# Optimization experiments

Measured on AMD Instinct MI355X. Metric: run time of the kernel, lower is better.

## Reference

```python
import jax, jax.numpy as jnp
import numpy as np

B, T, D_IN, D_OUT, N_HEAD = 2, 2048, 1024, 1024, 16
HEAD_DIM = D_OUT // N_HEAD


def setup_inputs() -> dict:
    key = jax.random.key(0)
    k1, k2, k3, k4 = jax.random.split(key, 4)
    s = 0.02  # init scale for weights
    return {
        "x": jax.random.normal(k1, (B, T, D_IN), jnp.float32),
        "Wq": jax.random.normal(k2, (D_OUT, D_IN), jnp.float32) * s,
        "Wk": jax.random.normal(k3, (D_OUT, D_IN), jnp.float32) * s,
        "Wv": jax.random.normal(k4, (D_OUT, D_IN), jnp.float32) * s,
    }


def reference(x, Wq, Wk, Wv):
    b, t, _ = x.shape
    h, hd = N_HEAD, HEAD_DIM
    # Linear projections (torch Linear: x @ W.T), split heads -> [b,h,t,hd]
    q = (x @ Wq.T).reshape(b, t, h, hd).transpose(0, 2, 1, 3)
    k = (x @ Wk.T).reshape(b, t, h, hd).transpose(0, 2, 1, 3)
    v = (x @ Wv.T).reshape(b, t, h, hd).transpose(0, 2, 1, 3)
    # raw scores [b,h,t,t], causal mask BEFORE scaling (as in source)
    omega = jnp.einsum("bhqd,bhkd->bhqk", q, k)
    causal = jnp.triu(jnp.ones((t, t), dtype=bool), k=1)
    omega = jnp.where(causal, -jnp.inf, omega)
    attw = jax.nn.softmax(omega / jnp.sqrt(jnp.asarray(hd, omega.dtype)), axis=-1)
    ctx = jnp.einsum("bhqk,bhkd->bhqd", attw, v)  # [b,h,t,hd]
    # Faithful to source: transpose(2,3) then view(B,T,d_out)
    out = jnp.swapaxes(ctx, 2, 3).reshape(b, t, D_OUT)
    return out
```

## Files before the change

kernel.cpp:

```cpp
#include <hip/hip_runtime.h>
#include <hip/hip_bf16.h>
#include <stdint.h>

typedef __attribute__((ext_vector_type(8))) short s16x8;
typedef __attribute__((ext_vector_type(4))) float f32x4;

#define T_   2048
#define NH   16
#define HD   64
#define DIN  1024
#define SCALE_LOG2 0.18033688011112042f

__device__ __forceinline__ unsigned short f2bf(float f) {
  union { float f; uint32_t u; } c; c.f = f;
  uint32_t u = c.u;
  return (unsigned short)((u + 0x7FFFu + ((u >> 16) & 1u)) >> 16);
}

__device__ __forceinline__ uint32_t pk_bf16(float a, float b) {
  __hip_bfloat162 h = __float22bfloat162_rn(make_float2(a, b));
  return *reinterpret_cast<uint32_t*>(&h);
}

#define GLL(gp, lp) __builtin_amdgcn_global_load_lds( \
    (__attribute__((address_space(1))) void*)(gp),    \
    (__attribute__((address_space(3))) void*)(lp), 16, 0, 0)

__global__ __launch_bounds__(256) void cvt_kernel(
    const float* __restrict__ x,  const float* __restrict__ wq,
    const float* __restrict__ wk, const float* __restrict__ wv,
    unsigned short* __restrict__ xb, unsigned short* __restrict__ wb) {
  int i = (blockIdx.x * 256 + threadIdx.x) * 4;
  float4 v;
  unsigned short* dp;
  if (i < 4194304) {
    v = *(const float4*)(x + i);
    dp = xb + i;
  } else {
    int j = i - 4194304;
    int seg = j >> 20, r = j & 1048575;
    const float* w = (seg == 0) ? wq : (seg == 1) ? wk : wv;
    v = *(const float4*)(w + r);
    dp = wb + j;
  }
  ushort4 o;
  o.x = f2bf(v.x); o.y = f2bf(v.y); o.z = f2bf(v.z); o.w = f2bf(v.w);
  *(ushort4*)dp = o;
}

__global__ __launch_bounds__(256) void qkv_gemm(
    const unsigned short* __restrict__ A, const unsigned short* __restrict__ Bm,
    unsigned short* __restrict__ qkv) {
  __shared__ __attribute__((aligned(16))) unsigned short Alds[128 * 64];
  __shared__ __attribute__((aligned(16))) unsigned short Blds[128 * 64];
  const int tid = threadIdx.x;
  const int lane = tid & 63, wave = tid >> 6;
  const int wm = wave >> 1, wn = wave & 1;
  const int m0 = blockIdx.y * 128, n0 = blockIdx.x * 128;

  f32x4 acc[4][4] = {};

  const int srow = wave * 32 + (lane >> 3);
  const int scol = (((lane & 7) ^ ((lane >> 3) & 7))) * 8;
  const unsigned short* ag = A  + (size_t)(m0 + srow) * DIN + scol;
  const unsigned short* bg = Bm + (size_t)(n0 + srow) * DIN + scol;
  unsigned short* al = &Alds[wave * 32 * 64];
  unsigned short* bl = &Blds[wave * 32 * 64];

  const int l16 = lane & 15, quad = lane >> 4;
  const int sw = l16 & 7;

  for (int k0 = 0; k0 < DIN; k0 += 64) {
    __syncthreads();
#pragma unroll
    for (int i = 0; i < 4; i++) {
      GLL(ag + (size_t)i * 8 * DIN + k0, al + i * 512);
      GLL(bg + (size_t)i * 8 * DIN + k0, bl + i * 512);
    }
    __syncthreads();
#pragma unroll
    for (int ks = 0; ks < 2; ks++) {
      const int cl = ((ks * 4 + quad) ^ sw) * 8;
      s16x8 af[4], bf[4];
#pragma unroll
      for (int mt = 0; mt < 4; mt++)
        af[mt] = *(const s16x8*)&Alds[(wm * 64 + mt * 16 + l16) * 64 + cl];
#pragma unroll
      for (int nt = 0; nt < 4; nt++)
        bf[nt] = *(const s16x8*)&Blds[(wn * 64 + nt * 16 + l16) * 64 + cl];
#pragma unroll
      for (int mt = 0; mt < 4; mt++)
#pragma unroll
        for (int nt = 0; nt < 4; nt++)
          acc[mt][nt] = __builtin_amdgcn_mfma_f32_16x16x32_bf16(af[mt], bf[nt], acc[mt][nt], 0, 0, 0);
    }
  }

#pragma unroll
  for (int mt = 0; mt < 4; mt++) {
    int mbase = m0 + wm * 64 + mt * 16 + (quad << 2);
    int b = mbase >> 11, t = mbase & 2047;
#pragma unroll
    for (int nt = 0; nt < 4; nt++) {
      int n = n0 + wn * 64 + nt * 16 + l16;
      int sel = n >> 10, h = (n >> 6) & 15, d = n & 63;
      int bh = b * NH + h;
      if (sel == 2) {
        ushort4 pk;
        pk.x = f2bf(acc[mt][nt][0]); pk.y = f2bf(acc[mt][nt][1]);
        pk.z = f2bf(acc[mt][nt][2]); pk.w = f2bf(acc[mt][nt][3]);
        *(ushort4*)&qkv[8388608 + (size_t)(bh * HD + d) * T_ + t] = pk;
      } else {
        float qs = (sel == 0) ? SCALE_LOG2 : 1.f;
#pragma unroll
        for (int r = 0; r < 4; r++)
          qkv[(size_t)sel * 4194304 + (size_t)(bh * T_ + t + r) * HD + d] =
              f2bf(acc[mt][nt][r] * qs);
      }
    }
  }
}

__global__ __launch_bounds__(256) void attn_kernel(
    const unsigned short* __restrict__ qkv, float* __restrict__ out) {
  __shared__ __attribute__((aligned(16))) unsigned short Klds[64 * 64];
  __shared__ __attribute__((aligned(16))) unsigned short Vt[64 * 64];
  __shared__ __attribute__((aligned(16))) unsigned short Plds[64 * 64];

  const int lane = threadIdx.x & 63, wave = threadIdx.x >> 6;
  const int l16 = lane & 15, quad = lane >> 4;
  const int swl = l16 & 7;
  const int qt = 31 - blockIdx.y, bh = blockIdx.x;
  const int q0 = qt * 64;
  const size_t bh_off = (size_t)bh * (T_ * HD);
  const unsigned short* Q  = qkv;
  const unsigned short* Kb = qkv + 4194304 + bh_off;
  const unsigned short* Vb = qkv + 8388608 + bh_off;

  s16x8 qf[2];
  {
    const unsigned short* qp =
        Q + bh_off + (size_t)(q0 + wave * 16 + l16) * HD + quad * 8;
    qf[0] = *(const s16x8*)(qp);
    qf[1] = *(const s16x8*)(qp + 32);
  }

  const int sr = threadIdx.x >> 3;
  const int sc = (threadIdx.x & 7) * 8;
  const int swc = (((threadIdx.x & 7) ^ (sr & 7))) * 8;

  s16x8 kr0 = *(const s16x8*)&Kb[(size_t)sr * HD + sc];
  s16x8 kr1 = *(const s16x8*)&Kb[(size_t)(sr + 32) * HD + sc];
  s16x8 vr0 = *(const s16x8*)&Vb[(size_t)sr * T_ + sc];
  s16x8 vr1 = *(const s16x8*)&Vb[(size_t)(sr + 32) * T_ + sc];

  const s16x8 onesf = {0x3F80, 0x3F80, 0x3F80, 0x3F80,
                       0x3F80, 0x3F80, 0x3F80, 0x3F80};
  f32x4 o[4] = {};
  f32x4 lacc = {};

  uint32_t* prow = (uint32_t*)&Plds[(wave * 16 + l16) * 64];
  const unsigned short* prd = &Plds[(wave * 16 + l16) * 64];

  for (int kt = 0; kt <= qt; kt++) {
    __syncthreads();
    *(s16x8*)&Klds[sr * 64 + swc] = kr0;
    *(s16x8*)&Klds[(sr + 32) * 64 + swc] = kr1;
    *(s16x8*)&Vt[sr * 64 + swc] = vr0;
    *(s16x8*)&Vt[(sr + 32) * 64 + swc] = vr1;
    if (kt < qt) {
      const unsigned short* kp = Kb + (size_t)(kt + 1) * 64 * HD;
      const unsigned short* vp = Vb + (kt + 1) * 64;
      kr0 = *(const s16x8*)&kp[(size_t)sr * HD + sc];
      kr1 = *(const s16x8*)&kp[(size_t)(sr + 32) * HD + sc];
      vr0 = *(const s16x8*)&vp[(size_t)sr * T_ + sc];
      vr1 = *(const s16x8*)&vp[(size_t)(sr + 32) * T_ + sc];
    }
    __syncthreads();

    f32x4 s[4] = {};
#pragma unroll
    for (int kk = 0; kk < 2; kk++) {
      const int cl = ((kk * 4 + quad) ^ swl) * 8;
#pragma unroll
      for (int nt = 0; nt < 4; nt++) {
        s16x8 kf = *(const s16x8*)&Klds[(nt * 16 + l16) * 64 + cl];
        s[nt] = __builtin_amdgcn_mfma_f32_16x16x32_bf16(kf, qf[kk], s[nt], 0, 0, 0);
      }
    }

    if (kt < qt) {
#pragma unroll
      for (int nt = 0; nt < 4; nt++) {
        float p0 = exp2f(s[nt][0]);
        float p1 = exp2f(s[nt][1]);
        float p2 = exp2f(s[nt][2]);
        float p3 = exp2f(s[nt][3]);
        *(uint2*)&prow[(((2 * nt + (quad >> 1)) ^ swl) << 2) + (quad & 1) * 2] =
            make_uint2(pk_bf16(p0, p1), pk_bf16(p2, p3));
      }
    } else {
      const int lim = wave * 16 + l16;
#pragma unroll
      for (int nt = 0; nt < 4; nt++) {
        const int kb = nt * 16 + quad * 4;
        float p0 = (kb + 0 <= lim) ? exp2f(s[nt][0]) : 0.f;
        float p1 = (kb + 1 <= lim) ? exp2f(s[nt][1]) : 0.f;
        float p2 = (kb + 2 <= lim) ? exp2f(s[nt][2]) : 0.f;
        float p3 = (kb + 3 <= lim) ? exp2f(s[nt][3]) : 0.f;
        *(uint2*)&prow[(((2 * nt + (quad >> 1)) ^ swl) << 2) + (quad & 1) * 2] =
            make_uint2(pk_bf16(p0, p1), pk_bf16(p2, p3));
      }
    }

#pragma unroll
    for (int kk = 0; kk < 2; kk++) {
      const int cl = ((kk * 4 + quad) ^ swl) * 8;
      s16x8 pf = *(const s16x8*)&prd[cl];
      lacc = __builtin_amdgcn_mfma_f32_16x16x32_bf16(pf, onesf, lacc, 0, 0, 0);
#pragma unroll
      for (int dt = 0; dt < 4; dt++) {
        s16x8 vf = *(const s16x8*)&Vt[(dt * 16 + l16) * 64 + cl];
        o[dt] = __builtin_amdgcn_mfma_f32_16x16x32_bf16(pf, vf, o[dt], 0, 0, 0);
      }
    }
  }

  f32x4 inv;
#pragma unroll
  for (int r = 0; r < 4; r++) inv[r] = 1.f / lacc[r];
#pragma unroll
  for (int dt = 0; dt < 4; dt++) {
    float4 v = make_float4(o[dt][0] * inv[0], o[dt][1] * inv[1],
                           o[dt][2] * inv[2], o[dt][3] * inv[3]);
    *(float4*)(out + (size_t)bh * (HD * T_) + (size_t)(dt * 16 + l16) * T_ +
               q0 + wave * 16 + quad * 4) = v;
  }
}

extern "C" void kernel_launch(void* const* d_in, const int* in_sizes, int n_in,
                              void* d_out, int out_size, void* d_ws, size_t ws_size,
                              hipStream_t stream) {
  const float* x  = (const float*)d_in[0];
  const float* wq = (const float*)d_in[1];
  const float* wk = (const float*)d_in[2];
  const float* wv = (const float*)d_in[3];
  float* out = (float*)d_out;

  unsigned short* xb  = (unsigned short*)d_ws;
  unsigned short* wb  = xb + 4194304;
  unsigned short* qkv = wb + 3145728;

  cvt_kernel<<<7168, 256, 0, stream>>>(x, wq, wk, wv, xb, wb);
  dim3 g1(24, 32);
  qkv_gemm<<<g1, 256, 0, stream>>>(xb, wb, qkv);
  dim3 g2(32, 32);
  attn_kernel<<<g2, 256, 0, stream>>>(qkv, out);
}
```

Baseline: 152.5 us.

## Split attention keys across waves and keep P in registers

Restructures the attention kernel so each wave owns a 16-key slice of every key tile and computes scores for all 64 queries. K fragments now load straight from global into registers, and the probabilities stay in registers as zero-padded MFMA operands, so the K and P LDS round-trips go away. Each wave's partial outputs and row sums are then summed across waves through shared memory at the end. In exchange, the padded operands waste half of each PV and row-sum MFMA, the MFMA count per tile rises, and the final cross-wave reduction adds LDS traffic and barriers.

```diff
diff --git a/kernel.cpp b/kernel.cpp
--- a/kernel.cpp
+++ b/kernel.cpp
@@ -3,6 +3,7 @@
 #include <stdint.h>
 
 typedef __attribute__((ext_vector_type(8))) short s16x8;
+typedef __attribute__((ext_vector_type(4))) short s16x4;
 typedef __attribute__((ext_vector_type(4))) float f32x4;
 
 #define T_   2048
@@ -10,6 +11,8 @@
 #define HD   64
 #define DIN  1024
 #define SCALE_LOG2 0.18033688011112042f
+
+#define MFMA32(a, b, c) __builtin_amdgcn_mfma_f32_16x16x32_bf16(a, b, c, 0, 0, 0)
 
 __device__ __forceinline__ unsigned short f2bf(float f) {
   union { float f; uint32_t u; } c; c.f = f;
@@ -92,7 +95,7 @@
       for (int mt = 0; mt < 4; mt++)
 #pragma unroll
         for (int nt = 0; nt < 4; nt++)
-          acc[mt][nt] = __builtin_amdgcn_mfma_f32_16x16x32_bf16(af[mt], bf[nt], acc[mt][nt], 0, 0, 0);
+          acc[mt][nt] = MFMA32(af[mt], bf[nt], acc[mt][nt]);
     }
   }
 
@@ -123,56 +126,51 @@
 
 __global__ __launch_bounds__(256) void attn_kernel(
     const unsigned short* __restrict__ qkv, float* __restrict__ out) {
-  __shared__ __attribute__((aligned(16))) unsigned short Klds[64 * 64];
-  __shared__ __attribute__((aligned(16))) unsigned short Vt[64 * 64];
-  __shared__ __attribute__((aligned(16))) unsigned short Plds[64 * 64];
+  __shared__ __attribute__((aligned(16))) unsigned char smem[28672];
+  unsigned short* Vt = (unsigned short*)smem;
+  float* Red = (float*)smem;
+  float* Lred = (float*)(smem + 24576);
 
   const int lane = threadIdx.x & 63, wave = threadIdx.x >> 6;
   const int l16 = lane & 15, quad = lane >> 4;
-  const int swl = l16 & 7;
   const int qt = 31 - blockIdx.y, bh = blockIdx.x;
   const int q0 = qt * 64;
   const size_t bh_off = (size_t)bh * (T_ * HD);
-  const unsigned short* Q  = qkv;
+  const unsigned short* Q  = qkv + bh_off;
   const unsigned short* Kb = qkv + 4194304 + bh_off;
   const unsigned short* Vb = qkv + 8388608 + bh_off;
 
-  s16x8 qf[2];
-  {
-    const unsigned short* qp =
-        Q + bh_off + (size_t)(q0 + wave * 16 + l16) * HD + quad * 8;
-    qf[0] = *(const s16x8*)(qp);
-    qf[1] = *(const s16x8*)(qp + 32);
+  s16x8 qf[4][2];
+#pragma unroll
+  for (int nq = 0; nq < 4; nq++) {
+    const unsigned short* qp = Q + (size_t)(q0 + nq * 16 + l16) * HD + quad * 8;
+    qf[nq][0] = *(const s16x8*)(qp);
+    qf[nq][1] = *(const s16x8*)(qp + 32);
   }
 
   const int sr = threadIdx.x >> 3;
   const int sc = (threadIdx.x & 7) * 8;
   const int swc = (((threadIdx.x & 7) ^ (sr & 7))) * 8;
 
-  s16x8 kr0 = *(const s16x8*)&Kb[(size_t)sr * HD + sc];
-  s16x8 kr1 = *(const s16x8*)&Kb[(size_t)(sr + 32) * HD + sc];
   s16x8 vr0 = *(const s16x8*)&Vb[(size_t)sr * T_ + sc];
   s16x8 vr1 = *(const s16x8*)&Vb[(size_t)(sr + 32) * T_ + sc];
-
-  const s16x8 onesf = {0x3F80, 0x3F80, 0x3F80, 0x3F80,
+  const unsigned short* kp0 = Kb + (size_t)(wave * 16 + l16) * HD + quad * 8;
+  s16x8 kf0 = *(const s16x8*)(kp0);
+  s16x8 kf1 = *(const s16x8*)(kp0 + 32);
+
+  const s16x8 ones8 = {0x3F80, 0x3F80, 0x3F80, 0x3F80,
                        0x3F80, 0x3F80, 0x3F80, 0x3F80};
-  f32x4 o[4] = {};
-  f32x4 lacc = {};
-
-  uint32_t* prow = (uint32_t*)&Plds[(wave * 16 + l16) * 64];
-  const unsigned short* prd = &Plds[(wave * 16 + l16) * 64];
+  f32x4 o[4][4] = {};
+  f32x4 lacc[4] = {};
+
+  const int vchunk = (((2 * wave + (quad >> 1)) ^ (l16 & 7)) << 3) + (quad & 1) * 4;
 
   for (int kt = 0; kt <= qt; kt++) {
     __syncthreads();
-    *(s16x8*)&Klds[sr * 64 + swc] = kr0;
-    *(s16x8*)&Klds[(sr + 32) * 64 + swc] = kr1;
     *(s16x8*)&Vt[sr * 64 + swc] = vr0;
     *(s16x8*)&Vt[(sr + 32) * 64 + swc] = vr1;
     if (kt < qt) {
-      const unsigned short* kp = Kb + (size_t)(kt + 1) * 64 * HD;
       const unsigned short* vp = Vb + (kt + 1) * 64;
-      kr0 = *(const s16x8*)&kp[(size_t)sr * HD + sc];
-      kr1 = *(const s16x8*)&kp[(size_t)(sr + 32) * HD + sc];
       vr0 = *(const s16x8*)&vp[(size_t)sr * T_ + sc];
       vr1 = *(const s16x8*)&vp[(size_t)(sr + 32) * T_ + sc];
     }
@@ -180,61 +178,109 @@
 
     f32x4 s[4] = {};
 #pragma unroll
-    for (int kk = 0; kk < 2; kk++) {
-      const int cl = ((kk * 4 + quad) ^ swl) * 8;
-#pragma unroll
-      for (int nt = 0; nt < 4; nt++) {
-        s16x8 kf = *(const s16x8*)&Klds[(nt * 16 + l16) * 64 + cl];
-        s[nt] = __builtin_amdgcn_mfma_f32_16x16x32_bf16(kf, qf[kk], s[nt], 0, 0, 0);
-      }
-    }
-
+    for (int nq = 0; nq < 4; nq++) {
+      s[nq] = MFMA32(kf0, qf[nq][0], s[nq]);
+      s[nq] = MFMA32(kf1, qf[nq][1], s[nq]);
+    }
     if (kt < qt) {
-#pragma unroll
-      for (int nt = 0; nt < 4; nt++) {
-        float p0 = exp2f(s[nt][0]);
-        float p1 = exp2f(s[nt][1]);
-        float p2 = exp2f(s[nt][2]);
-        float p3 = exp2f(s[nt][3]);
-        *(uint2*)&prow[(((2 * nt + (quad >> 1)) ^ swl) << 2) + (quad & 1) * 2] =
-            make_uint2(pk_bf16(p0, p1), pk_bf16(p2, p3));
+      const unsigned short* kp =
+          Kb + (size_t)((kt + 1) * 64 + wave * 16 + l16) * HD + quad * 8;
+      kf0 = *(const s16x8*)(kp);
+      kf1 = *(const s16x8*)(kp + 32);
+    }
+
+    s16x8 pf[4];
+    if (kt < qt) {
+#pragma unroll
+      for (int nq = 0; nq < 4; nq++) {
+        float p0 = exp2f(s[nq][0]);
+        float p1 = exp2f(s[nq][1]);
+        float p2 = exp2f(s[nq][2]);
+        float p3 = exp2f(s[nq][3]);
+        union { s16x8 v; uint4 u; } pu;
+        pu.u = make_uint4(pk_bf16(p0, p1), pk_bf16(p2, p3), 0u, 0u);
+        pf[nq] = pu.v;
       }
     } else {
-      const int lim = wave * 16 + l16;
-#pragma unroll
-      for (int nt = 0; nt < 4; nt++) {
-        const int kb = nt * 16 + quad * 4;
-        float p0 = (kb + 0 <= lim) ? exp2f(s[nt][0]) : 0.f;
-        float p1 = (kb + 1 <= lim) ? exp2f(s[nt][1]) : 0.f;
-        float p2 = (kb + 2 <= lim) ? exp2f(s[nt][2]) : 0.f;
-        float p3 = (kb + 3 <= lim) ? exp2f(s[nt][3]) : 0.f;
-        *(uint2*)&prow[(((2 * nt + (quad >> 1)) ^ swl) << 2) + (quad & 1) * 2] =
-            make_uint2(pk_bf16(p0, p1), pk_bf16(p2, p3));
-      }
-    }
-
-#pragma unroll
-    for (int kk = 0; kk < 2; kk++) {
-      const int cl = ((kk * 4 + quad) ^ swl) * 8;
-      s16x8 pf = *(const s16x8*)&prd[cl];
-      lacc = __builtin_amdgcn_mfma_f32_16x16x32_bf16(pf, onesf, lacc, 0, 0, 0);
-#pragma unroll
-      for (int dt = 0; dt < 4; dt++) {
-        s16x8 vf = *(const s16x8*)&Vt[(dt * 16 + l16) * 64 + cl];
-        o[dt] = __builtin_amdgcn_mfma_f32_16x16x32_bf16(pf, vf, o[dt], 0, 0, 0);
-      }
-    }
-  }
-
-  f32x4 inv;
-#pragma unroll
-  for (int r = 0; r < 4; r++) inv[r] = 1.f / lacc[r];
-#pragma unroll
-  for (int dt = 0; dt < 4; dt++) {
-    float4 v = make_float4(o[dt][0] * inv[0], o[dt][1] * inv[1],
-                           o[dt][2] * inv[2], o[dt][3] * inv[3]);
-    *(float4*)(out + (size_t)bh * (HD * T_) + (size_t)(dt * 16 + l16) * T_ +
-               q0 + wave * 16 + quad * 4) = v;
+#pragma unroll
+      for (int nq = 0; nq < 4; nq++) {
+        const int lim = nq * 16 + l16 - wave * 16 - quad * 4;
+        float p0 = (0 <= lim) ? exp2f(s[nq][0]) : 0.f;
+        float p1 = (1 <= lim) ? exp2f(s[nq][1]) : 0.f;
+        float p2 = (2 <= lim) ? exp2f(s[nq][2]) : 0.f;
+        float p3 = (3 <= lim) ? exp2f(s[nq][3]) : 0.f;
+        union { s16x8 v; uint4 u; } pu;
+        pu.u = make_uint4(pk_bf16(p0, p1), pk_bf16(p2, p3), 0u, 0u);
+        pf[nq] = pu.v;
+      }
+    }
+
+#pragma unroll
+    for (int mq = 0; mq < 4; mq++)
+      lacc[mq] = MFMA32(pf[mq], ones8, lacc[mq]);
+#pragma unroll
+    for (int nd = 0; nd < 4; nd++) {
+      s16x4 vf4 = *(const s16x4*)&Vt[(nd * 16 + l16) * 64 + vchunk];
+      s16x8 vf = {vf4[0], vf4[1], vf4[2], vf4[3], 0, 0, 0, 0};
+#pragma unroll
+      for (int mq = 0; mq < 4; mq++)
+        o[mq][nd] = MFMA32(pf[mq], vf, o[mq][nd]);
+    }
+  }
+
+  __syncthreads();
+  if (l16 == 0) {
+#pragma unroll
+    for (int mq = 0; mq < 4; mq++)
+      *(f32x4*)&Lred[wave * 64 + mq * 16 + quad * 4] = lacc[mq];
+  }
+
+  f32x4 osum[4];
+#pragma unroll
+  for (int nd = 0; nd < 4; nd++)
+    if (nd == wave) {
+#pragma unroll
+      for (int mq = 0; mq < 4; mq++) osum[mq] = o[mq][nd];
+    }
+
+#pragma unroll
+  for (int half = 0; half < 2; half++) {
+    const int mqA = half * 2, mqB = half * 2 + 1;
+#pragma unroll
+    for (int nd = 0; nd < 4; nd++) {
+      if (nd != wave) {
+        const int reg = nd * 3 + (wave > nd ? wave - 1 : wave);
+        float* wr = Red + reg * 512 + lane * 8;
+        *(f32x4*)&wr[0] = o[mqA][nd];
+        *(f32x4*)&wr[4] = o[mqB][nd];
+      }
+    }
+    __syncthreads();
+#pragma unroll
+    for (int v = 0; v < 4; v++) {
+      if (v != wave) {
+        const int reg = wave * 3 + (v > wave ? v - 1 : v);
+        const float* rd = Red + reg * 512 + lane * 8;
+        osum[mqA] += *(const f32x4*)&rd[0];
+        osum[mqB] += *(const f32x4*)&rd[4];
+      }
+    }
+    __syncthreads();
+  }
+
+#pragma unroll
+  for (int mq = 0; mq < 4; mq++) {
+    f32x4 lt = {};
+#pragma unroll
+    for (int v = 0; v < 4; v++)
+      lt += *(const f32x4*)&Lred[v * 64 + mq * 16 + quad * 4];
+    float4 res;
+    res.x = osum[mq][0] / lt[0];
+    res.y = osum[mq][1] / lt[1];
+    res.z = osum[mq][2] / lt[2];
+    res.w = osum[mq][3] / lt[3];
+    *(float4*)(out + (size_t)bh * (HD * T_) + (size_t)(wave * 16 + l16) * T_ +
+               q0 + mq * 16 + quad * 4) = res;
   }
 }
 
```

Measured after the change: 163.7 us. 1.07x slower.

## Split attention query tiles to 32 rows with two-wave blocks

Applied to the files above, without the earlier changes.

The attention kernel now gives each block 32 query rows handled by two waves instead of 64 rows handled by four, doubling the grid to 2048 blocks. The K/V tile load is spread over 128 threads with four loads each, and the causal mask is generalised to partial-diagonal tiles. The goal is better load balance and occupancy across CUs for the triangular workload. The cost is more redundant K/V global loads per query row, since each 64-key tile is now fetched by twice as many blocks, plus more barrier overhead per unit of work.

```diff
diff --git a/kernel.cpp b/kernel.cpp
--- a/kernel.cpp
+++ b/kernel.cpp
@@ -10,6 +10,8 @@
 #define HD   64
 #define DIN  1024
 #define SCALE_LOG2 0.18033688011112042f
+
+#define MFMA32(a, b, c) __builtin_amdgcn_mfma_f32_16x16x32_bf16(a, b, c, 0, 0, 0)
 
 __device__ __forceinline__ unsigned short f2bf(float f) {
   union { float f; uint32_t u; } c; c.f = f;
@@ -92,7 +94,7 @@
       for (int mt = 0; mt < 4; mt++)
 #pragma unroll
         for (int nt = 0; nt < 4; nt++)
-          acc[mt][nt] = __builtin_amdgcn_mfma_f32_16x16x32_bf16(af[mt], bf[nt], acc[mt][nt], 0, 0, 0);
+          acc[mt][nt] = MFMA32(af[mt], bf[nt], acc[mt][nt]);
     }
   }
 
@@ -121,26 +123,27 @@
   }
 }
 
-__global__ __launch_bounds__(256) void attn_kernel(
+__global__ __launch_bounds__(128) void attn_kernel(
     const unsigned short* __restrict__ qkv, float* __restrict__ out) {
   __shared__ __attribute__((aligned(16))) unsigned short Klds[64 * 64];
   __shared__ __attribute__((aligned(16))) unsigned short Vt[64 * 64];
-  __shared__ __attribute__((aligned(16))) unsigned short Plds[64 * 64];
+  __shared__ __attribute__((aligned(16))) unsigned short Plds[2 * 16 * 64];
 
   const int lane = threadIdx.x & 63, wave = threadIdx.x >> 6;
   const int l16 = lane & 15, quad = lane >> 4;
   const int swl = l16 & 7;
-  const int qt = 31 - blockIdx.y, bh = blockIdx.x;
-  const int q0 = qt * 64;
+  const int qt = 63 - blockIdx.y, bh = blockIdx.x;
+  const int q0 = qt * 32;
+  const int qw = q0 + wave * 16;
+  const int ktmax = (q0 + 31) >> 6;
   const size_t bh_off = (size_t)bh * (T_ * HD);
-  const unsigned short* Q  = qkv;
+  const unsigned short* Q  = qkv + bh_off;
   const unsigned short* Kb = qkv + 4194304 + bh_off;
   const unsigned short* Vb = qkv + 8388608 + bh_off;
 
   s16x8 qf[2];
   {
-    const unsigned short* qp =
-        Q + bh_off + (size_t)(q0 + wave * 16 + l16) * HD + quad * 8;
+    const unsigned short* qp = Q + (size_t)(qw + l16) * HD + quad * 8;
     qf[0] = *(const s16x8*)(qp);
     qf[1] = *(const s16x8*)(qp + 32);
   }
@@ -149,10 +152,12 @@
   const int sc = (threadIdx.x & 7) * 8;
   const int swc = (((threadIdx.x & 7) ^ (sr & 7))) * 8;
 
-  s16x8 kr0 = *(const s16x8*)&Kb[(size_t)sr * HD + sc];
-  s16x8 kr1 = *(const s16x8*)&Kb[(size_t)(sr + 32) * HD + sc];
-  s16x8 vr0 = *(const s16x8*)&Vb[(size_t)sr * T_ + sc];
-  s16x8 vr1 = *(const s16x8*)&Vb[(size_t)(sr + 32) * T_ + sc];
+  s16x8 kr[4], vr[4];
+#pragma unroll
+  for (int i = 0; i < 4; i++) {
+    kr[i] = *(const s16x8*)&Kb[(size_t)(sr + 16 * i) * HD + sc];
+    vr[i] = *(const s16x8*)&Vb[(size_t)(sr + 16 * i) * T_ + sc];
+  }
 
   const s16x8 onesf = {0x3F80, 0x3F80, 0x3F80, 0x3F80,
                        0x3F80, 0x3F80, 0x3F80, 0x3F80};
@@ -162,19 +167,21 @@
   uint32_t* prow = (uint32_t*)&Plds[(wave * 16 + l16) * 64];
   const unsigned short* prd = &Plds[(wave * 16 + l16) * 64];
 
-  for (int kt = 0; kt <= qt; kt++) {
-    __syncthreads();
-    *(s16x8*)&Klds[sr * 64 + swc] = kr0;
-    *(s16x8*)&Klds[(sr + 32) * 64 + swc] = kr1;
-    *(s16x8*)&Vt[sr * 64 + swc] = vr0;
-    *(s16x8*)&Vt[(sr + 32) * 64 + swc] = vr1;
-    if (kt < qt) {
+  for (int kt = 0; kt <= ktmax; kt++) {
+    __syncthreads();
+#pragma unroll
+    for (int i = 0; i < 4; i++) {
+      *(s16x8*)&Klds[(sr + 16 * i) * 64 + swc] = kr[i];
+      *(s16x8*)&Vt[(sr + 16 * i) * 64 + swc] = vr[i];
+    }
+    if (kt < ktmax) {
       const unsigned short* kp = Kb + (size_t)(kt + 1) * 64 * HD;
       const unsigned short* vp = Vb + (kt + 1) * 64;
-      kr0 = *(const s16x8*)&kp[(size_t)sr * HD + sc];
-      kr1 = *(const s16x8*)&kp[(size_t)(sr + 32) * HD + sc];
-      vr0 = *(const s16x8*)&vp[(size_t)sr * T_ + sc];
-      vr1 = *(const s16x8*)&vp[(size_t)(sr + 32) * T_ + sc];
+#pragma unroll
+      for (int i = 0; i < 4; i++) {
+        kr[i] = *(const s16x8*)&kp[(size_t)(sr + 16 * i) * HD + sc];
+        vr[i] = *(const s16x8*)&vp[(size_t)(sr + 16 * i) * T_ + sc];
+      }
     }
     __syncthreads();
 
@@ -185,11 +192,11 @@
 #pragma unroll
       for (int nt = 0; nt < 4; nt++) {
         s16x8 kf = *(const s16x8*)&Klds[(nt * 16 + l16) * 64 + cl];
-        s[nt] = __builtin_amdgcn_mfma_f32_16x16x32_bf16(kf, qf[kk], s[nt], 0, 0, 0);
-      }
-    }
-
-    if (kt < qt) {
+        s[nt] = MFMA32(kf, qf[kk], s[nt]);
+      }
+    }
+
+    if (kt * 64 + 63 <= qw) {
 #pragma unroll
       for (int nt = 0; nt < 4; nt++) {
         float p0 = exp2f(s[nt][0]);
@@ -200,7 +207,7 @@
             make_uint2(pk_bf16(p0, p1), pk_bf16(p2, p3));
       }
     } else {
-      const int lim = wave * 16 + l16;
+      const int lim = qw + l16 - kt * 64;
 #pragma unroll
       for (int nt = 0; nt < 4; nt++) {
         const int kb = nt * 16 + quad * 4;
@@ -217,11 +224,11 @@
     for (int kk = 0; kk < 2; kk++) {
       const int cl = ((kk * 4 + quad) ^ swl) * 8;
       s16x8 pf = *(const s16x8*)&prd[cl];
-      lacc = __builtin_amdgcn_mfma_f32_16x16x32_bf16(pf, onesf, lacc, 0, 0, 0);
+      lacc = MFMA32(pf, onesf, lacc);
 #pragma unroll
       for (int dt = 0; dt < 4; dt++) {
         s16x8 vf = *(const s16x8*)&Vt[(dt * 16 + l16) * 64 + cl];
-        o[dt] = __builtin_amdgcn_mfma_f32_16x16x32_bf16(pf, vf, o[dt], 0, 0, 0);
+        o[dt] = MFMA32(pf, vf, o[dt]);
       }
     }
   }
@@ -234,7 +241,7 @@
     float4 v = make_float4(o[dt][0] * inv[0], o[dt][1] * inv[1],
                            o[dt][2] * inv[2], o[dt][3] * inv[3]);
     *(float4*)(out + (size_t)bh * (HD * T_) + (size_t)(dt * 16 + l16) * T_ +
-               q0 + wave * 16 + quad * 4) = v;
+               qw + quad * 4) = v;
   }
 }
 
@@ -254,6 +261,6 @@
   cvt_kernel<<<7168, 256, 0, stream>>>(x, wq, wk, wv, xb, wb);
   dim3 g1(24, 32);
   qkv_gemm<<<g1, 256, 0, stream>>>(xb, wb, qkv);
-  dim3 g2(32, 32);
-  attn_kernel<<<g2, 256, 0, stream>>>(qkv, out);
-}
+  dim3 g2(32, 64);
+  attn_kernel<<<g2, 128, 0, stream>>>(qkv, out);
+}
```

Result: slower. 163.1 us (+7.0%).
